# Kernel tuning notes

Hardware: AMD Instinct MI355X
Metric: run time of the kernel (lower is better)

## Reference

```python
import jax, jax.numpy as jnp
import numpy as np

E = 5          # number of experts / candidate encoders
NSUB = 13      # subband axis from x.reshape([B, 13, -1])


def _complex_corr_mean(y, y_):
    # y: [E, B, 13, F] (interleaved re/im), y_: [B, 13, F]
    ai, aj = y[..., 0::2], y[..., 1::2]        # [E,B,13,F/2]
    bi, bj = y_[..., 0::2], y_[..., 1::2]      # [B,13,F/2]
    i = (ai * bi + aj * bj).sum(-1)            # [E,B,13]
    j = (ai * bj - aj * bi).sum(-1)            # [E,B,13]
    c = i * i + j * j                          # |<a, conj(b)>|^2 per subband
    return c.mean(-1)                          # [E,B]


def setup_inputs() -> dict:
    key = jax.random.key(0)
    k = jax.random.split(key, 5)
    B, F, D = 4096, 9984, 512
    return {
        "x": jax.random.normal(k[0], (B, F), dtype=jnp.float32),
        "W_enc": jax.random.normal(k[1], (E, F, D), dtype=jnp.float32) * 0.02,
        "b_enc": jnp.zeros((E, D), dtype=jnp.float32),
        "W_dec": jax.random.normal(k[2], (E, D, F), dtype=jnp.float32) * 0.02,
        "b_dec": jnp.zeros((E, F), dtype=jnp.float32),
    }


def reference(x, W_enc, b_enc, W_dec, b_dec):
    B = x.shape[0]
    # per-expert encode: out[e] = encoder_e(x) -> latent code [E, B, D]
    out = jnp.einsum("bf,efd->ebd", x, W_enc) + b_enc[:, None, :]
    # per-expert decode: y[e] = decoder_e(out[e]) -> reconstruction [E, B, F]
    y = jnp.einsum("ebd,edf->ebf", out, W_dec) + b_dec[:, None, :]
    y = y.reshape(E, B, NSUB, -1)
    y_ = x.reshape(B, NSUB, -1)
    scores = _complex_corr_mean(y, y_)         # [E, B]
    idx = jnp.argmax(scores, axis=0)           # [B] best expert per sample
    # batch_gather: pick the winning expert's latent per sample
    sel = out[idx, jnp.arange(B)]              # [B, D]
    return sel
```

## Files before the change

### kernel.cpp

```cpp
#include <hip/hip_runtime.h>

#define E_ 5
#define B_ 4096
#define F_ 9984
#define D_ 512
#define NSUB_ 13
#define SUBW_ 768

typedef _Float16 f16;
typedef __attribute__((ext_vector_type(4))) _Float16 f16x4;
typedef __attribute__((ext_vector_type(8))) _Float16 f16x8;
typedef __attribute__((ext_vector_type(16))) float f32x16;

#define BK 32
#define PLANE_H 4096
#define BUF_H   16384

__device__ __forceinline__ int swz(int row, int c) {
    return row * BK + ((c ^ ((row >> 1) & 3)) << 3);
}

struct Pf { f16x8 v[8]; };

__device__ __forceinline__ void loadPf(Pf& pf,
        const f16* __restrict__ Ah, const f16* __restrict__ Al, int sA,
        const f16* __restrict__ Bh, const f16* __restrict__ Bl, int sB,
        int k0, int row, int cb) {
    const size_t ra = (size_t)row * sA + k0 + cb * 8;
    const size_t rb = (size_t)row * sB + k0 + cb * 8;
    pf.v[0] = *(const f16x8*)(Ah + ra);
    pf.v[1] = *(const f16x8*)(Ah + ra + 8);
    pf.v[2] = *(const f16x8*)(Al + ra);
    pf.v[3] = *(const f16x8*)(Al + ra + 8);
    pf.v[4] = *(const f16x8*)(Bh + rb);
    pf.v[5] = *(const f16x8*)(Bh + rb + 8);
    pf.v[6] = *(const f16x8*)(Bl + rb);
    pf.v[7] = *(const f16x8*)(Bl + rb + 8);
}

__device__ __forceinline__ void writePf(f16* L, const Pf& pf, int row, int cb) {
    const int o0 = swz(row, cb), o1 = swz(row, cb + 1);
    *(f16x8*)(L + 0*PLANE_H + o0) = pf.v[0];
    *(f16x8*)(L + 0*PLANE_H + o1) = pf.v[1];
    *(f16x8*)(L + 1*PLANE_H + o0) = pf.v[2];
    *(f16x8*)(L + 1*PLANE_H + o1) = pf.v[3];
    *(f16x8*)(L + 2*PLANE_H + o0) = pf.v[4];
    *(f16x8*)(L + 2*PLANE_H + o1) = pf.v[5];
    *(f16x8*)(L + 3*PLANE_H + o0) = pf.v[6];
    *(f16x8*)(L + 3*PLANE_H + o1) = pf.v[7];
}

#define MFMA(a, b, c) __builtin_amdgcn_mfma_f32_32x32x16_f16((a), (b), (c), 0, 0, 0)

__device__ __forceinline__ void computeK(const f16* L,
        int rA0, int kA0, int rA1, int kA1,
        int rB0, int kB0, int rB1, int kB1, int g,
        f32x16 accm[2][2], f32x16 accx[2][2]) {
    #pragma unroll
    for (int sub = 0; sub < 2; ++sub) {
        const int c = sub * 2 + g;
        f16x8 ah0 = *(const f16x8*)(L + 0*PLANE_H + rA0 + (((c ^ kA0)) << 3));
        f16x8 ah1 = *(const f16x8*)(L + 0*PLANE_H + rA1 + (((c ^ kA1)) << 3));
        f16x8 al0 = *(const f16x8*)(L + 1*PLANE_H + rA0 + (((c ^ kA0)) << 3));
        f16x8 al1 = *(const f16x8*)(L + 1*PLANE_H + rA1 + (((c ^ kA1)) << 3));
        f16x8 bh0 = *(const f16x8*)(L + 2*PLANE_H + rB0 + (((c ^ kB0)) << 3));
        f16x8 bh1 = *(const f16x8*)(L + 2*PLANE_H + rB1 + (((c ^ kB1)) << 3));
        f16x8 bl0 = *(const f16x8*)(L + 3*PLANE_H + rB0 + (((c ^ kB0)) << 3));
        f16x8 bl1 = *(const f16x8*)(L + 3*PLANE_H + rB1 + (((c ^ kB1)) << 3));
        accm[0][0] = MFMA(ah0, bh0, accm[0][0]);
        accm[0][1] = MFMA(ah0, bh1, accm[0][1]);
        accm[1][0] = MFMA(ah1, bh0, accm[1][0]);
        accm[1][1] = MFMA(ah1, bh1, accm[1][1]);
        accx[0][0] = MFMA(ah0, bl0, accx[0][0]);
        accx[0][0] = MFMA(al0, bh0, accx[0][0]);
        accx[0][1] = MFMA(ah0, bl1, accx[0][1]);
        accx[0][1] = MFMA(al0, bh1, accx[0][1]);
        accx[1][0] = MFMA(ah1, bl0, accx[1][0]);
        accx[1][0] = MFMA(al1, bh0, accx[1][0]);
        accx[1][1] = MFMA(ah1, bl1, accx[1][1]);
        accx[1][1] = MFMA(al1, bh1, accx[1][1]);
    }
}

__device__ __forceinline__ void gemm_core2(
    const f16* __restrict__ Ah, const f16* __restrict__ Al, int sA,
    const f16* __restrict__ Bh, const f16* __restrict__ Bl, int sB,
    int nk, f16* lds, int t, int wm, int wn, int l31, int g,
    f32x16 accm[2][2], f32x16 accx[2][2])
{
    const int row = t >> 1, cb = (t & 1) * 2;
    const int rowA0 = wm + l31,      rowA1 = wm + 32 + l31;
    const int rowB0 = wn + l31,      rowB1 = wn + 32 + l31;
    const int rA0 = rowA0 * BK, kA0 = (rowA0 >> 1) & 3;
    const int rA1 = rowA1 * BK, kA1 = (rowA1 >> 1) & 3;
    const int rB0 = rowB0 * BK, kB0 = (rowB0 >> 1) & 3;
    const int rB1 = rowB1 * BK, kB1 = (rowB1 >> 1) & 3;

    Pf pf;
    loadPf(pf, Ah, Al, sA, Bh, Bl, sB, 0, row, cb);
    writePf(lds, pf, row, cb);
    asm volatile("s_waitcnt lgkmcnt(0)" ::: "memory");
    __builtin_amdgcn_s_barrier();
    __builtin_amdgcn_sched_barrier(0);

    for (int kt = 0; kt < nk; ++kt) {
        const bool more = (kt + 1 < nk);
        if (more) loadPf(pf, Ah, Al, sA, Bh, Bl, sB, (kt + 1) * BK, row, cb);
        const f16* L = lds + (kt & 1) * BUF_H;
        computeK(L, rA0, kA0, rA1, kA1, rB0, kB0, rB1, kB1, g, accm, accx);
        if (more) writePf(lds + ((kt + 1) & 1) * BUF_H, pf, row, cb);
        asm volatile("s_waitcnt lgkmcnt(0)" ::: "memory");
        __builtin_amdgcn_s_barrier();
        __builtin_amdgcn_sched_barrier(0);
    }
}

__global__ __launch_bounds__(256) void split_x(const float* __restrict__ x,
                                               f16* __restrict__ xhi, f16* __restrict__ xlo) {
    size_t i = ((size_t)blockIdx.x * 256 + threadIdx.x) * 4;
    float4 v = *(const float4*)&x[i];
    float vv[4] = {v.x, v.y, v.z, v.w};
    f16x4 h, l;
    #pragma unroll
    for (int k = 0; k < 4; ++k) {
        f16 hh = (f16)vv[k];
        h[k] = hh;
        l[k] = (f16)((vv[k] - (float)hh) * 2048.0f);
    }
    *(f16x4*)&xhi[i] = h;
    *(f16x4*)&xlo[i] = l;
}

__global__ __launch_bounds__(256) void splitT_W(const float* __restrict__ W,
                                                f16* __restrict__ Thi, f16* __restrict__ Tlo,
                                                int R, int C) {
    __shared__ float tile[64][65];
    const int rt = blockIdx.x, ct = blockIdx.y, e = blockIdx.z;
    const int t = threadIdx.x;
    const int r0 = rt * 64, c0 = ct * 64;
    const int tr = t >> 4, tc4 = (t & 15) * 4;
    const float* Wp = W + (size_t)e * R * C;
    #pragma unroll
    for (int p = 0; p < 4; ++p) {
        float4 v = *(const float4*)&Wp[(size_t)(r0 + tr + p*16) * C + c0 + tc4];
        tile[tr + p*16][tc4 + 0] = v.x;
        tile[tr + p*16][tc4 + 1] = v.y;
        tile[tr + p*16][tc4 + 2] = v.z;
        tile[tr + p*16][tc4 + 3] = v.w;
    }
    __syncthreads();
    f16* Th = Thi + (size_t)e * R * C;
    f16* Tl = Tlo + (size_t)e * R * C;
    #pragma unroll
    for (int p = 0; p < 4; ++p) {
        const int cr = tr + p*16;
        f16x4 h, l;
        #pragma unroll
        for (int k = 0; k < 4; ++k) {
            float v = tile[tc4 + k][cr] * 64.0f;
            f16 hh = (f16)v;
            h[k] = hh;
            l[k] = (f16)((v - (float)hh) * 2048.0f);
        }
        size_t off = (size_t)(c0 + cr) * R + r0 + tc4;
        *(f16x4*)&Th[off] = h;
        *(f16x4*)&Tl[off] = l;
    }
}

__global__ __launch_bounds__(256, 2) void mm_enc2(
    const f16* __restrict__ xhi, const f16* __restrict__ xlo,
    const f16* __restrict__ wthi, const f16* __restrict__ wtlo,
    const float* __restrict__ bias, int Kloc,
    f16* __restrict__ outHi, f16* __restrict__ outLo)
{
    __shared__ f16 lds[2 * BUF_H];
    const int de = blockIdx.x;
    const int bt = blockIdx.y;
    const int ks = blockIdx.z;
    const int dt = de & 3, e = de >> 2;
    const int koff = ks * Kloc;
    const int t = threadIdx.x, lane = t & 63, l31 = lane & 31, g = lane >> 5, wid = t >> 6;
    const int wm = (wid >> 1) * 64, wn = (wid & 1) * 64;
    const f16* Ah = xhi + (size_t)bt * 128 * F_ + koff;
    const f16* Al = xlo + (size_t)bt * 128 * F_ + koff;
    const f16* Bh = wthi + ((size_t)e * D_ + dt * 128) * F_ + koff;
    const f16* Bl = wtlo + ((size_t)e * D_ + dt * 128) * F_ + koff;
    f32x16 accm[2][2] = {}, accx[2][2] = {};
    gemm_core2(Ah, Al, F_, Bh, Bl, F_, Kloc / BK, lds, t, wm, wn, l31, g, accm, accx);

    f16* oH = outHi + (size_t)ks * E_ * B_ * D_;
    f16* oL = outLo + (size_t)ks * E_ * B_ * D_;
    #pragma unroll
    for (int fn = 0; fn < 2; ++fn) {
        const int d = dt * 128 + wn + fn * 32 + l31;
        const float be = bias ? bias[e * D_ + d] : 0.0f;
        #pragma unroll
        for (int fm = 0; fm < 2; ++fm) {
            #pragma unroll
            for (int r = 0; r < 16; ++r) {
                float v = (accm[fm][fn][r] + accx[fm][fn][r] * (1.0f/2048.0f)) * (1.0f/64.0f) + be;
                int brow = bt * 128 + wm + fm * 32 + (r & 3) + 8 * (r >> 2) + 4 * g;
                size_t off = ((size_t)e * B_ + brow) * D_ + d;
                f16 h = (f16)v;
                oH[off] = h;
                oL[off] = (f16)((v - (float)h) * 2048.0f);
            }
        }
    }
}

__global__ __launch_bounds__(256) void combine_k(
    const f16* __restrict__ pH, const f16* __restrict__ pL,
    const float* __restrict__ b_enc,
    f16* __restrict__ oH, f16* __restrict__ oL)
{
    const size_t NP = (size_t)E_ * B_ * D_;
    size_t i = ((size_t)blockIdx.x * 256 + threadIdx.x) * 8;
    f16x8 h0 = *(const f16x8*)(pH + i);
    f16x8 l0 = *(const f16x8*)(pL + i);
    f16x8 h1 = *(const f16x8*)(pH + NP + i);
    f16x8 l1 = *(const f16x8*)(pL + NP + i);
    const int d = (int)(i % D_);
    const int e = (int)(i / ((size_t)B_ * D_));
    f16x8 oh, ol;
    #pragma unroll
    for (int k = 0; k < 8; ++k) {
        float v = (float)h0[k] + (float)l0[k] * (1.0f/2048.0f)
                + (float)h1[k] + (float)l1[k] * (1.0f/2048.0f)
                + b_enc[e * D_ + d + k];
        f16 hh = (f16)v;
        oh[k] = hh;
        ol[k] = (f16)((v - (float)hh) * 2048.0f);
    }
    *(f16x8*)&oH[i] = oh;
    *(f16x8*)&oL[i] = ol;
}

__global__ __launch_bounds__(256, 2) void mm_dec2(
    const f16* __restrict__ wthi, const f16* __restrict__ wtlo,
    const f16* __restrict__ ohi, const f16* __restrict__ olo,
    const float* __restrict__ b_dec, const float* __restrict__ x,
    float* __restrict__ ijbuf)
{
    __shared__ f16 lds[2 * BUF_H];
    const int se = blockIdx.x;
    const int e = se % 5, s = se / 5;
    const int ft = blockIdx.y, bt = blockIdx.z;
    const int t = threadIdx.x, lane = t & 63, l31 = lane & 31, g = lane >> 5, wid = t >> 6;
    const int wm = (wid >> 1) * 64, wn = (wid & 1) * 64;
    const int f0blk = s * SUBW_ + ft * 128;
    const f16* Ah = wthi + ((size_t)e * F_ + f0blk) * D_;
    const f16* Al = wtlo + ((size_t)e * F_ + f0blk) * D_;
    const f16* Bh = ohi + ((size_t)e * B_ + bt * 128) * D_;
    const f16* Bl = olo + ((size_t)e * B_ + bt * 128) * D_;
    f32x16 accm[2][2] = {}, accx[2][2] = {};
    gemm_core2(Ah, Al, D_, Bh, Bl, D_, D_ / BK, lds, t, wm, wn, l31, g, accm, accx);

    float ia[2] = {0.f, 0.f}, ja[2] = {0.f, 0.f};
    #pragma unroll
    for (int fm = 0; fm < 2; ++fm) {
        #pragma unroll
        for (int q = 0; q < 8; ++q) {
            const int r = q * 2;
            const int fg = f0blk + wm + fm * 32 + (r & 3) + 8 * (r >> 2) + 4 * g;
            const float2 bd = *(const float2*)&b_dec[(size_t)e * F_ + fg];
            #pragma unroll
            for (int fn = 0; fn < 2; ++fn) {
                const int b = bt * 128 + wn + fn * 32 + l31;
                const float2 xv = *(const float2*)&x[(size_t)b * F_ + fg];
                float y0 = (accm[fm][fn][r]     + accx[fm][fn][r]     * (1.0f/2048.0f)) * (1.0f/64.0f) + bd.x;
                float y1 = (accm[fm][fn][r + 1] + accx[fm][fn][r + 1] * (1.0f/2048.0f)) * (1.0f/64.0f) + bd.y;
                ia[fn] += y0 * xv.x + y1 * xv.y;
                ja[fn] += y0 * xv.y - y1 * xv.x;
            }
        }
    }
    #pragma unroll
    for (int fn = 0; fn < 2; ++fn) {
        ia[fn] += __shfl_xor(ia[fn], 32, 64);
        ja[fn] += __shfl_xor(ja[fn], 32, 64);
    }
    float* red = (float*)lds;
    const int wr = wid >> 1, wc = wid & 1;
    if (wr == 0 && lane < 32) {
        #pragma unroll
        for (int fn = 0; fn < 2; ++fn) {
            red[(wc * 64 + fn * 32 + l31) * 2 + 0] = ia[fn];
            red[(wc * 64 + fn * 32 + l31) * 2 + 1] = ja[fn];
        }
    }
    __syncthreads();
    if (wr == 1 && lane < 32) {
        #pragma unroll
        for (int fn = 0; fn < 2; ++fn) {
            float gi = ia[fn] + red[(wc * 64 + fn * 32 + l31) * 2 + 0];
            float gj = ja[fn] + red[(wc * 64 + fn * 32 + l31) * 2 + 1];
            int b = bt * 128 + wc * 64 + fn * 32 + l31;
            size_t base = (((size_t)(e * NSUB_ + s)) * 6 + ft) * 2;
            ijbuf[(base + 0) * B_ + b] = gi;
            ijbuf[(base + 1) * B_ + b] = gj;
        }
    }
}

__global__ __launch_bounds__(256) void argmax2(const float* __restrict__ ijbuf, int* __restrict__ idx) {
    int b = blockIdx.x * 256 + threadIdx.x;
    float best = -1.0f; int bi = 0;
    for (int e = 0; e < E_; ++e) {
        float sc = 0.f;
        for (int s = 0; s < NSUB_; ++s) {
            float ii = 0.f, jj = 0.f;
            #pragma unroll
            for (int ft = 0; ft < 6; ++ft) {
                size_t base = (((size_t)(e * NSUB_ + s)) * 6 + ft) * 2;
                ii += ijbuf[base * B_ + b];
                jj += ijbuf[(base + 1) * B_ + b];
            }
            sc += ii * ii + jj * jj;
        }
        if (sc > best) { best = sc; bi = e; }
    }
    idx[b] = bi;
}

__global__ __launch_bounds__(256) void gather2(const f16* __restrict__ outHi, const f16* __restrict__ outLo,
                                               const int* __restrict__ idx, float* __restrict__ sel) {
    int tg = blockIdx.x * 256 + threadIdx.x;
    int b = tg >> 7, dq = (tg & 127) * 4;
    int e = idx[b];
    size_t off = ((size_t)e * B_ + b) * D_ + dq;
    f16x4 h = *(const f16x4*)&outHi[off];
    f16x4 l = *(const f16x4*)&outLo[off];
    float4 o;
    o.x = (float)h[0] + (float)l[0] * (1.0f/2048.0f);
    o.y = (float)h[1] + (float)l[1] * (1.0f/2048.0f);
    o.z = (float)h[2] + (float)l[2] * (1.0f/2048.0f);
    o.w = (float)h[3] + (float)l[3] * (1.0f/2048.0f);
    *(float4*)&sel[(size_t)b * D_ + dq] = o;
}

__global__ __launch_bounds__(256) void enc_gemm(const float* __restrict__ x,
                                                const float* __restrict__ W_enc,
                                                const float* __restrict__ b_enc,
                                                float* __restrict__ out)
{
    __shared__ float As[16][68];
    __shared__ float Bs[16][68];
    const int btile = blockIdx.x;
    const int en    = blockIdx.y;
    const int e  = en >> 3;
    const int n0 = (en & 7) * 64;
    const int b0 = btile * 64;
    const int tid = threadIdx.x;
    const int tx = tid & 15, ty = tid >> 4;
    const float* Wp = W_enc + (size_t)e * F_ * D_;
    const int arow = tid >> 2;
    const int ac4  = (tid & 3) * 4;
    const int bk   = tid >> 4;
    const int bn   = (tid & 15) * 4;
    float acc[4][4] = {};
    for (int k0 = 0; k0 < F_; k0 += 16) {
        float4 av = *(const float4*)&x[(size_t)(b0 + arow) * F_ + k0 + ac4];
        As[ac4 + 0][arow] = av.x; As[ac4 + 1][arow] = av.y;
        As[ac4 + 2][arow] = av.z; As[ac4 + 3][arow] = av.w;
        float4 bv = *(const float4*)&Wp[(size_t)(k0 + bk) * D_ + n0 + bn];
        *(float4*)&Bs[bk][bn] = bv;
        __syncthreads();
        #pragma unroll
        for (int k = 0; k < 16; ++k) {
            float4 a = *(const float4*)&As[k][ty * 4];
            float4 b = *(const float4*)&Bs[k][tx * 4];
            float ar[4] = {a.x, a.y, a.z, a.w};
            float br[4] = {b.x, b.y, b.z, b.w};
            #pragma unroll
            for (int r = 0; r < 4; ++r)
                #pragma unroll
                for (int c = 0; c < 4; ++c)
                    acc[r][c] += ar[r] * br[c];
        }
        __syncthreads();
    }
    float4 be = *(const float4*)&b_enc[e * D_ + n0 + tx * 4];
    #pragma unroll
    for (int r = 0; r < 4; ++r) {
        int b = b0 + ty * 4 + r;
        float4 o;
        o.x = acc[r][0] + be.x; o.y = acc[r][1] + be.y;
        o.z = acc[r][2] + be.z; o.w = acc[r][3] + be.w;
        *(float4*)&out[((size_t)e * B_ + b) * D_ + n0 + tx * 4] = o;
    }
}

__global__ __launch_bounds__(256) void dec_score(const float* __restrict__ out,
                                                 const float* __restrict__ W_dec,
                                                 const float* __restrict__ b_dec,
                                                 const float* __restrict__ x,
                                                 float* __restrict__ cbuf)
{
    __shared__ float As[16][68];
    __shared__ float Bs[16][68];
    const int btile = blockIdx.x;
    const int es    = blockIdx.y;
    const int e = es / 13;
    const int s = es % 13;
    const int b0 = btile * 64;
    const int fbase = s * SUBW_;
    const int tid = threadIdx.x;
    const int tx = tid & 15, ty = tid >> 4;
    const float* Ap = out   + (size_t)e * B_ * D_;
    const float* Wp = W_dec + (size_t)e * D_ * F_;
    const int arow = tid >> 2;
    const int ac4  = (tid & 3) * 4;
    const int bk   = tid >> 4;
    const int bn   = (tid & 15) * 4;
    float ip[4] = {}, jp[4] = {};
    for (int u = 0; u < 12; ++u) {
        const int f0 = fbase + u * 64;
        float acc[4][4] = {};
        for (int k0 = 0; k0 < D_; k0 += 16) {
            float4 av = *(const float4*)&Ap[(size_t)(b0 + arow) * D_ + k0 + ac4];
            As[ac4 + 0][arow] = av.x; As[ac4 + 1][arow] = av.y;
            As[ac4 + 2][arow] = av.z; As[ac4 + 3][arow] = av.w;
            float4 bv = *(const float4*)&Wp[(size_t)(k0 + bk) * F_ + f0 + bn];
            *(float4*)&Bs[bk][bn] = bv;
            __syncthreads();
            #pragma unroll
            for (int k = 0; k < 16; ++k) {
                float4 a = *(const float4*)&As[k][ty * 4];
                float4 b = *(const float4*)&Bs[k][tx * 4];
                float ar[4] = {a.x, a.y, a.z, a.w};
                float br[4] = {b.x, b.y, b.z, b.w};
                #pragma unroll
                for (int r = 0; r < 4; ++r)
                    #pragma unroll
                    for (int c = 0; c < 4; ++c)
                        acc[r][c] += ar[r] * br[c];
            }
            __syncthreads();
        }
        float4 bd = *(const float4*)&b_dec[(size_t)e * F_ + f0 + tx * 4];
        #pragma unroll
        for (int r = 0; r < 4; ++r) {
            int b = b0 + ty * 4 + r;
            float4 xv = *(const float4*)&x[(size_t)b * F_ + f0 + tx * 4];
            float y0 = acc[r][0] + bd.x;
            float y1 = acc[r][1] + bd.y;
            float y2 = acc[r][2] + bd.z;
            float y3 = acc[r][3] + bd.w;
            ip[r] += y0 * xv.x + y1 * xv.y + y2 * xv.z + y3 * xv.w;
            jp[r] += y0 * xv.y - y1 * xv.x + y2 * xv.w - y3 * xv.z;
        }
    }
    #pragma unroll
    for (int r = 0; r < 4; ++r) {
        float iv = ip[r], jv = jp[r];
        #pragma unroll
        for (int m = 1; m < 16; m <<= 1) {
            iv += __shfl_xor(iv, m, 64);
            jv += __shfl_xor(jv, m, 64);
        }
        if (tx == 0) {
            int b = b0 + ty * 4 + r;
            cbuf[((size_t)e * B_ + b) * NSUB_ + s] = iv * iv + jv * jv;
        }
    }
}

__global__ __launch_bounds__(256) void argmax_k(const float* __restrict__ cbuf,
                                                int* __restrict__ idx)
{
    int b = blockIdx.x * blockDim.x + threadIdx.x;
    if (b >= B_) return;
    float best = -1e30f;
    int bi = 0;
    for (int e = 0; e < E_; ++e) {
        float ssum = 0.f;
        #pragma unroll
        for (int s = 0; s < NSUB_; ++s)
            ssum += cbuf[((size_t)e * B_ + b) * NSUB_ + s];
        if (ssum > best) { best = ssum; bi = e; }
    }
    idx[b] = bi;
}

__global__ __launch_bounds__(256) void gather_k(const float* __restrict__ out,
                                                const int* __restrict__ idx,
                                                float* __restrict__ sel)
{
    int t = blockIdx.x * blockDim.x + threadIdx.x;
    int b = t >> 7;
    int c = (t & 127) * 4;
    int e = idx[b];
    *(float4*)&sel[(size_t)b * D_ + c] =
        *(const float4*)&out[((size_t)e * B_ + b) * D_ + c];
}

extern "C" void kernel_launch(void* const* d_in, const int* in_sizes, int n_in,
                              void* d_out, int out_size, void* d_ws, size_t ws_size,
                              hipStream_t stream)
{
    const float* x     = (const float*)d_in[0];
    const float* W_enc = (const float*)d_in[1];
    const float* b_enc = (const float*)d_in[2];
    const float* W_dec = (const float*)d_in[3];
    const float* b_dec = (const float*)d_in[4];
    float* sel = (float*)d_out;

    const size_t szXplane = (size_t)B_ * F_ * sizeof(f16);
    const size_t szWplane = (size_t)E_ * F_ * D_ * sizeof(f16);
    const size_t szOplane = (size_t)E_ * B_ * D_ * sizeof(f16);
    const size_t szIJ     = (size_t)E_ * NSUB_ * 6 * 2 * B_ * sizeof(float);
    const size_t need      = 2*szXplane + 2*szWplane + 2*szOplane + szIJ + (size_t)B_*4;
    const size_t needSplit = need + 4*szOplane;

    if (ws_size >= need) {
        char* p = (char*)d_ws;
        f16* xhi  = (f16*)p; p += szXplane;
        f16* xlo  = (f16*)p; p += szXplane;
        f16* wthi = (f16*)p; p += szWplane;
        f16* wtlo = (f16*)p; p += szWplane;
        f16* ohi  = (f16*)p; p += szOplane;
        f16* olo  = (f16*)p; p += szOplane;
        float* ij = (float*)p; p += szIJ;
        int* idx  = (int*)p; p += (size_t)B_*4;

        split_x<<<39936, 256, 0, stream>>>(x, xhi, xlo);
        splitT_W<<<dim3(F_/64, D_/64, E_), 256, 0, stream>>>(W_enc, wthi, wtlo, F_, D_);

        if (ws_size >= needSplit) {
            f16* pH = (f16*)p; p += 2*szOplane;
            f16* pL = (f16*)p;
            mm_enc2<<<dim3(20, 32, 2), 256, 0, stream>>>(xhi, xlo, wthi, wtlo,
                                                         nullptr, F_/2, pH, pL);
            combine_k<<<(E_*B_*D_)/(8*256), 256, 0, stream>>>(pH, pL, b_enc, ohi, olo);
        } else {
            mm_enc2<<<dim3(20, 32, 1), 256, 0, stream>>>(xhi, xlo, wthi, wtlo,
                                                         b_enc, F_, ohi, olo);
        }
        splitT_W<<<dim3(D_/64, F_/64, E_), 256, 0, stream>>>(W_dec, wthi, wtlo, D_, F_);
        mm_dec2<<<dim3(65, 6, 32), 256, 0, stream>>>(wthi, wtlo, ohi, olo, b_dec, x, ij);
        argmax2<<<16, 256, 0, stream>>>(ij, idx);
        gather2<<<2048, 256, 0, stream>>>(ohi, olo, idx, sel);
    } else {
        float* out  = (float*)d_ws;
        float* cbuf = out + (size_t)E_ * B_ * D_;
        int*   idx  = (int*)(cbuf + (size_t)E_ * B_ * NSUB_);
        enc_gemm <<<dim3(64, 40), 256, 0, stream>>>(x, W_enc, b_enc, out);
        dec_score<<<dim3(64, 65), 256, 0, stream>>>(out, W_dec, b_dec, x, cbuf);
        argmax_k <<<dim3(B_ / 256), 256, 0, stream>>>(cbuf, idx);
        gather_k <<<dim3(B_ * D_ / 4 / 256), 256, 0, stream>>>(out, idx, sel);
    }
}
```

Measured before the change: 1.966 ms.

## Load GEMM tiles directly into LDS with global_load_lds, one plane per wave

Replaces the register-staged global-to-LDS tile copy in the shared GEMM core with direct global_load_lds transfers. Each wave now fills one of the four hi/lo A/B planes, with the XOR swizzle moved onto the global source address. Synchronisation switches to vmcnt waits plus two barriers per k-step. This frees staging registers and drops the VGPR-to-LDS write instructions, at the cost of an extra barrier per iteration and a tighter dependency on the load-wait ordering.

```diff
diff --git a/kernel.cpp b/kernel.cpp
--- a/kernel.cpp
+++ b/kernel.cpp
@@ -16,41 +16,13 @@
 #define PLANE_H 4096
 #define BUF_H   16384
 
-__device__ __forceinline__ int swz(int row, int c) {
-    return row * BK + ((c ^ ((row >> 1) & 3)) << 3);
-}
-
-struct Pf { f16x8 v[8]; };
-
-__device__ __forceinline__ void loadPf(Pf& pf,
-        const f16* __restrict__ Ah, const f16* __restrict__ Al, int sA,
-        const f16* __restrict__ Bh, const f16* __restrict__ Bl, int sB,
-        int k0, int row, int cb) {
-    const size_t ra = (size_t)row * sA + k0 + cb * 8;
-    const size_t rb = (size_t)row * sB + k0 + cb * 8;
-    pf.v[0] = *(const f16x8*)(Ah + ra);
-    pf.v[1] = *(const f16x8*)(Ah + ra + 8);
-    pf.v[2] = *(const f16x8*)(Al + ra);
-    pf.v[3] = *(const f16x8*)(Al + ra + 8);
-    pf.v[4] = *(const f16x8*)(Bh + rb);
-    pf.v[5] = *(const f16x8*)(Bh + rb + 8);
-    pf.v[6] = *(const f16x8*)(Bl + rb);
-    pf.v[7] = *(const f16x8*)(Bl + rb + 8);
-}
-
-__device__ __forceinline__ void writePf(f16* L, const Pf& pf, int row, int cb) {
-    const int o0 = swz(row, cb), o1 = swz(row, cb + 1);
-    *(f16x8*)(L + 0*PLANE_H + o0) = pf.v[0];
-    *(f16x8*)(L + 0*PLANE_H + o1) = pf.v[1];
-    *(f16x8*)(L + 1*PLANE_H + o0) = pf.v[2];
-    *(f16x8*)(L + 1*PLANE_H + o1) = pf.v[3];
-    *(f16x8*)(L + 2*PLANE_H + o0) = pf.v[4];
-    *(f16x8*)(L + 2*PLANE_H + o1) = pf.v[5];
-    *(f16x8*)(L + 3*PLANE_H + o0) = pf.v[6];
-    *(f16x8*)(L + 3*PLANE_H + o1) = pf.v[7];
-}
-
 #define MFMA(a, b, c) __builtin_amdgcn_mfma_f32_32x32x16_f16((a), (b), (c), 0, 0, 0)
+
+__device__ __forceinline__ void gload16(const f16* g, f16* l) {
+    __builtin_amdgcn_global_load_lds(
+        (const __attribute__((address_space(1))) void*)g,
+        (__attribute__((address_space(3))) void*)l, 16, 0, 0);
+}
 
 __device__ __forceinline__ void computeK(const f16* L,
         int rA0, int kA0, int rA1, int kA1,
@@ -82,13 +54,25 @@
     }
 }
 
-__device__ __forceinline__ void gemm_core2(
+__device__ __forceinline__ void gemm_core3(
     const f16* __restrict__ Ah, const f16* __restrict__ Al, int sA,
     const f16* __restrict__ Bh, const f16* __restrict__ Bl, int sB,
     int nk, f16* lds, int t, int wm, int wn, int l31, int g,
     f32x16 accm[2][2], f32x16 accx[2][2])
 {
-    const int row = t >> 1, cb = (t & 1) * 2;
+    const int lane = t & 63, wid = t >> 6;
+    const int lrow = lane >> 2, lch = lane & 3;
+    const f16* gp = (wid == 0) ? Ah : (wid == 1) ? Al : (wid == 2) ? Bh : Bl;
+    const int gs = (wid < 2) ? sA : sB;
+    f16* plane = lds + wid * PLANE_H;
+
+    size_t goff[8];
+    #pragma unroll
+    for (int s = 0; s < 8; ++s) {
+        const int row = s * 16 + lrow;
+        goff[s] = (size_t)row * gs + ((lch ^ ((row >> 1) & 3)) << 3);
+    }
+
     const int rowA0 = wm + l31,      rowA1 = wm + 32 + l31;
     const int rowB0 = wn + l31,      rowB1 = wn + 32 + l31;
     const int rA0 = rowA0 * BK, kA0 = (rowA0 >> 1) & 3;
@@ -96,20 +80,27 @@
     const int rB0 = rowB0 * BK, kB0 = (rowB0 >> 1) & 3;
     const int rB1 = rowB1 * BK, kB1 = (rowB1 >> 1) & 3;
 
-    Pf pf;
-    loadPf(pf, Ah, Al, sA, Bh, Bl, sB, 0, row, cb);
-    writePf(lds, pf, row, cb);
-    asm volatile("s_waitcnt lgkmcnt(0)" ::: "memory");
-    __builtin_amdgcn_s_barrier();
-    __builtin_amdgcn_sched_barrier(0);
+    #pragma unroll
+    for (int s = 0; s < 8; ++s)
+        gload16(gp + goff[s], plane + s * (16 * BK));
 
     for (int kt = 0; kt < nk; ++kt) {
         const bool more = (kt + 1 < nk);
-        if (more) loadPf(pf, Ah, Al, sA, Bh, Bl, sB, (kt + 1) * BK, row, cb);
+        if (more) {
+            f16* dst = plane + ((kt + 1) & 1) * BUF_H;
+            const int k0 = (kt + 1) * BK;
+            #pragma unroll
+            for (int s = 0; s < 8; ++s)
+                gload16(gp + goff[s] + k0, dst + s * (16 * BK));
+            asm volatile("s_waitcnt vmcnt(8)" ::: "memory");
+        } else {
+            asm volatile("s_waitcnt vmcnt(0)" ::: "memory");
+        }
+        __builtin_amdgcn_s_barrier();
+        __builtin_amdgcn_sched_barrier(0);
         const f16* L = lds + (kt & 1) * BUF_H;
         computeK(L, rA0, kA0, rA1, kA1, rB0, kB0, rB1, kB1, g, accm, accx);
-        if (more) writePf(lds + ((kt + 1) & 1) * BUF_H, pf, row, cb);
-        asm volatile("s_waitcnt lgkmcnt(0)" ::: "memory");
+        __builtin_amdgcn_sched_barrier(0);
         __builtin_amdgcn_s_barrier();
         __builtin_amdgcn_sched_barrier(0);
     }
@@ -187,7 +178,7 @@
     const f16* Bh = wthi + ((size_t)e * D_ + dt * 128) * F_ + koff;
     const f16* Bl = wtlo + ((size_t)e * D_ + dt * 128) * F_ + koff;
     f32x16 accm[2][2] = {}, accx[2][2] = {};
-    gemm_core2(Ah, Al, F_, Bh, Bl, F_, Kloc / BK, lds, t, wm, wn, l31, g, accm, accx);
+    gemm_core3(Ah, Al, F_, Bh, Bl, F_, Kloc / BK, lds, t, wm, wn, l31, g, accm, accx);
 
     f16* oH = outHi + (size_t)ks * E_ * B_ * D_;
     f16* oL = outLo + (size_t)ks * E_ * B_ * D_;
@@ -255,7 +246,7 @@
     const f16* Bh = ohi + ((size_t)e * B_ + bt * 128) * D_;
     const f16* Bl = olo + ((size_t)e * B_ + bt * 128) * D_;
     f32x16 accm[2][2] = {}, accx[2][2] = {};
-    gemm_core2(Ah, Al, D_, Bh, Bl, D_, D_ / BK, lds, t, wm, wn, l31, g, accm, accx);
+    gemm_core3(Ah, Al, D_, Bh, Bl, D_, D_ / BK, lds, t, wm, wn, l31, g, accm, accx);
 
     float ia[2] = {0.f, 0.f}, ja[2] = {0.f, 0.f};
     #pragma unroll
```

Result: faster. 1.792 ms (-8.8%).
